# Performance work log

Hardware: AMD Instinct MI355X
Metric: run time of the kernel (lower is better)

## Reference

```python
import jax, jax.numpy as jnp
import numpy as np
from jax import lax

NQ = 9          # num_qubits
K = 3           # basis_size
S = 16          # max_num_snapshots
H = 128         # hidden_size
B = 16          # batch
D = 2 ** NQ

# basis_reconstruction buffer = Pauli X, Y, Z (complex64), non-trainable
PAULI = jnp.array([[[0, 1], [1, 0]],
                   [[0, -1j], [1j, 0]],
                   [[1, 0], [0, -1]]], dtype=jnp.complex64)


def setup_inputs() -> dict:
    key = jax.random.key(0)
    ks = jax.random.split(key, 11)
    return {
        "snapshot": jax.random.normal(ks[0], (B, NQ), jnp.float32),
        "basis_comp_vector": jax.random.uniform(ks[1], (B, NQ, K), dtype=jnp.float32),
        "rho": jax.random.normal(ks[2], (B, 2) + (2,) * NQ, jnp.float32),
        "h0": jax.random.normal(ks[3], (B, H), jnp.float32),
        "c0": jax.random.normal(ks[4], (B, H), jnp.float32),
        "W_ih": jax.random.normal(ks[5], (4 * H, NQ + NQ * K), jnp.float32) * 0.1,
        "W_hh": jax.random.normal(ks[6], (4 * H, H), jnp.float32) * 0.1,
        "b_ih": jax.random.normal(ks[7], (4 * H,), jnp.float32) * 0.1,
        "b_hh": jax.random.normal(ks[8], (4 * H,), jnp.float32) * 0.1,
        "Wp": jax.random.normal(ks[9], (NQ, K, H), jnp.float32) * 0.1,
        "bp": jax.random.normal(ks[10], (NQ, K), jnp.float32) * 0.1,
    }


def _lstm_cell(x, h, c, W_ih, W_hh, b_ih, b_hh):
    g = x @ W_ih.T + h @ W_hh.T + b_ih + b_hh
    i, f, gg, o = jnp.split(g, 4, axis=-1)  # torch gate order i,f,g,o
    i, f, o = jax.nn.sigmoid(i), jax.nn.sigmoid(f), jax.nn.sigmoid(o)
    c = f * c + i * jnp.tanh(gg)
    return o * jnp.tanh(c), c


def _apply_1q(psi, M, i):
    """Apply per-batch 2x2 matrix M [B,2,2] to qubit i of psi [B]+[2]*NQ."""
    psi = jnp.moveaxis(psi, 1 + i, 1)
    sh = psi.shape
    out = jnp.einsum('bij,bjr->bir', M, psi.reshape(sh[0], 2, -1))
    return jnp.moveaxis(out.reshape(sh), 1, 1 + i)


def _take_snapshots(psi, a):
    """Vectorized take_snapshot: psi [B]+[2]*NQ complex, a [B,NQ,K] real (sqrt of probs).
    For each qubit build psi_plus/psi_minus projectors, record expectation
    s = <P+> - <P-> and collapse onto the (normalized) plus branch."""
    axs = tuple(range(1, NQ + 1))
    zeros = jnp.zeros(psi.shape[0], jnp.float32)
    ss = []
    for i in range(NQ):
        a1, a2, a3 = a[:, i, 0], a[:, i, 1], a[:, i, 2]
        an = jnp.sqrt(a1 * a1 + a2 * a2 + a3 * a3)
        nrm = 1.0 / jnp.sqrt(2.0 * an * (a3 + an))
        pp = jnp.stack([lax.complex(a3 + an, zeros), lax.complex(a1, a2)], axis=-1) * nrm[:, None]
        pm = jnp.stack([lax.complex(-a1, a2), lax.complex(a3 + an, zeros)], axis=-1) * nrm[:, None]
        Pp = pp[:, :, None] * jnp.conj(pp)[:, None, :]  # [B,2,2]
        Pm = pm[:, :, None] * jnp.conj(pm)[:, None, :]
        psi_p = _apply_1q(psi, Pp, i)
        psi_m = _apply_1q(psi, Pm, i)
        prob_p = jnp.sum(psi_p.real ** 2 + psi_p.imag ** 2, axis=axs)
        prob_m = jnp.sum(psi_m.real ** 2 + psi_m.imag ** 2, axis=axs)
        ss.append(prob_p - prob_m)
        psi = psi_p / jnp.sqrt(prob_p).reshape((-1,) + (1,) * NQ)  # collapse
    return jnp.stack(ss, axis=1)  # [B,NQ]


def _bkron(A, Bm):
    b, m, n = A.shape
    p, q = Bm.shape[1], Bm.shape[2]
    return (A[:, :, None, :, None] * Bm[:, None, :, None, :]).reshape(b, m * p, n * q)


def _forward(snapshot, basis_comp_vector, rho, h0, c0, W_ih, W_hh, b_ih, b_hh, Wp, bp):
    b = snapshot.shape[0]
    psi = lax.complex(rho[:, 0], rho[:, 1])  # [B]+[2]*NQ pure state
    x = jnp.concatenate([snapshot, basis_comp_vector.reshape(b, -1)], axis=-1)
    inputs = [x]
    h, c = h0, c0
    for _ in range(S - 1):
        h, c = _lstm_cell(x, h, c, W_ih, W_hh, b_ih, b_hh)
        probs = jax.nn.softmax(jnp.einsum('bh,nkh->bnk', h, Wp) + bp, axis=-1)
        amps = jnp.sqrt(probs)  # [B,NQ,K]
        snap = _take_snapshots(psi, amps)
        x = jnp.concatenate([snap, amps.reshape(b, -1)], axis=-1)
        inputs.append(x)
    # classical-shadow reconstruction, summed over snapshots
    I2 = jnp.eye(2, dtype=jnp.complex64)
    acc = jnp.zeros((b, D, D), jnp.complex64)
    last_bv = None
    for x in inputs:
        shadow = x[:, :NQ]                                   # [B,NQ]
        bv = x[:, NQ:].reshape(b, NQ, K)
        last_bv = bv
        basis = jnp.einsum('bnk,kij->bnij', bv.astype(jnp.complex64), PAULI)
        rho_q = (I2 + shadow[:, :, None, None].astype(jnp.complex64) * basis * 3.0) / 2.0
        r = rho_q[:, 0]
        for iq in range(1, NQ):
            r = _bkron(r, rho_q[:, iq])
        acc = acc + r
    rho_rec = acc / S
    out = jnp.stack([rho_rec.real, rho_rec.imag], axis=1)  # [B,2,D,D]
    return out, last_bv


def reference(snapshot, basis_comp_vector, rho, h0, c0, W_ih, W_hh, b_ih, b_hh, Wp, bp):
    return _forward(snapshot, basis_comp_vector, rho, h0, c0,
                    W_ih, W_hh, b_ih, b_hh, Wp, bp)
```

## Files before the change

kernel.cpp:

```cpp
#include <hip/hip_runtime.h>
#include <math.h>

#define NQ 9
#define KK 3
#define S 16
#define H 128
#define BB 16
#define D 512
#define DD (D*D)

typedef float vfloat4 __attribute__((ext_vector_type(4)));

__device__ __forceinline__ float sigf(float x){ return 1.f/(1.f + __expf(-x)); }
__device__ __forceinline__ float tanhfast(float x){
  float e = __expf(2.f*x);
  return 1.f - 2.f/(e + 1.f);
}
#define RCP(x)  __builtin_amdgcn_rcpf(x)
#define RSQ(x)  __builtin_amdgcn_rsqf(x)

#define DPP_ADD(x, ctrl, rmask) \
  x += __int_as_float(__builtin_amdgcn_update_dpp(0, __float_as_int(x), ctrl, rmask, 0xf, false))

__device__ __forceinline__ float wave_red_sum(float x) {
  DPP_ADD(x, 0x111, 0xf);
  DPP_ADD(x, 0x112, 0xf);
  DPP_ADD(x, 0x114, 0xf);
  DPP_ADD(x, 0x118, 0xf);
  DPP_ADD(x, 0x142, 0xa);
  DPP_ADD(x, 0x143, 0xc);
  return __int_as_float(__builtin_amdgcn_readlane(__float_as_int(x), 63));
}
#define RL(v, l) __int_as_float(__builtin_amdgcn_readlane(__float_as_int(v), (l)))
#define DPP_ROR(x, n) \
  __int_as_float(__builtin_amdgcn_update_dpp(0, __float_as_int(x), 0x120 + (n), 0xf, 0xf, false))

__device__ __forceinline__ float ghh_rl4(const float4 (&whh)[32],
                                         float h0v, float h1v, float bias) {
  float g0 = bias, g1 = 0.f, g2 = 0.f, g3 = 0.f;
  #pragma unroll
  for (int j = 0; j < 32; ++j) {
    float4 wv = whh[j];
    g0 += wv.x*RL(h0v, 2*j);
    g1 += wv.y*RL(h1v, 2*j);
    g2 += wv.z*RL(h0v, 2*j + 1);
    g3 += wv.w*RL(h1v, 2*j + 1);
  }
  return (g0 + g1) + (g2 + g3);
}

__global__ __launch_bounds__(512, 2)
void seq_kernel(const float* __restrict__ snapshot,
                const float* __restrict__ bcv,
                const float* __restrict__ rho,
                const float* __restrict__ h0,
                const float* __restrict__ c0,
                const float* __restrict__ W_ih,
                const float* __restrict__ W_hh,
                const float* __restrict__ b_ih,
                const float* __restrict__ b_hh,
                const float* __restrict__ Wp,
                const float* __restrict__ bp,
                float4* __restrict__ mats,
                float* __restrict__ last_bv)
{
  const int b    = blockIdx.x;
  const int tid  = threadIdx.x;
  const int lane = tid & 63;
  const int w    = tid >> 6;

  __shared__ __align__(16) float xh[36];
  __shared__ float gbuf[512];
  __shared__ float prj[27];

  float4 wih[9], whh[32];
  {
    const float4* wi = (const float4*)(W_ih + tid*36);
    #pragma unroll
    for (int k = 0; k < 9; ++k) wih[k] = wi[k];
    const float4* wh = (const float4*)(W_hh + tid*H);
    #pragma unroll
    for (int k = 0; k < 32; ++k) whh[k] = wh[k];
  }
  const float bias = b_ih[tid] + b_hh[tid];

  float2 wpv[4]; float bpv[4];
  #pragma unroll
  for (int i = 0; i < 4; ++i) {
    int u = (w >= 1) ? (w - 1) + 7*i : 99;
    if (u < 27) { wpv[i] = *(const float2*)(Wp + u*H + 2*lane); bpv[i] = bp[u]; }
    else        { wpv[i] = make_float2(0.f, 0.f); bpv[i] = 0.f; }
  }

  float cc0 = c0[b*H + 2*lane], cc1 = c0[b*H + 2*lane + 1];
  float h0v = h0[b*H + 2*lane], h1v = h0[b*H + 2*lane + 1];

  float pr0[8], pi0[8], norm0 = 0.f;
  if (w == 0) {
    #pragma unroll
    for (int j = 0; j < 8; ++j) {
      pr0[j] = rho[b*1024 + j*64 + lane];
      pi0[j] = rho[b*1024 + 512 + j*64 + lane];
    }
    float ls = 0.f;
    #pragma unroll
    for (int j = 0; j < 8; ++j) ls += pr0[j]*pr0[j] + pi0[j]*pi0[j];
    norm0 = wave_red_sum(ls);
  }

  if (tid < NQ)  xh[tid]      = snapshot[b*NQ + tid];
  if (tid < 27)  xh[NQ + tid] = bcv[b*27 + tid];
  if (tid < NQ) {
    float s  = snapshot[b*NQ + tid];
    float v0 = bcv[b*27 + tid*3];
    float v1 = bcv[b*27 + tid*3 + 1];
    float v2 = bcv[b*27 + tid*3 + 2];
    mats[(b*S + 0)*NQ + tid] = make_float4(
        0.5f*(1.f + 3.f*s*v2), 1.5f*s*v0, -1.5f*s*v1, 0.5f*(1.f - 3.f*s*v2));
  }
  __syncthreads();

  float ghh = ghh_rl4(whh, h0v, h1v, bias);

  for (int t = 1; t < S; ++t) {
    {
      const float4* x4 = (const float4*)xh;
      float g0 = ghh, g1 = 0.f, g2 = 0.f, g3 = 0.f;
      #pragma unroll
      for (int k = 0; k < 9; ++k) {
        float4 wv = wih[k], xv = x4[k];
        g0 += wv.x*xv.x; g1 += wv.y*xv.y; g2 += wv.z*xv.z; g3 += wv.w*xv.w;
      }
      gbuf[tid] = (g0 + g1) + (g2 + g3);
    }
    __syncthreads();

    {
      float2 gI = *(const float2*)(gbuf + 2*lane);
      float2 gF = *(const float2*)(gbuf + 128 + 2*lane);
      float2 gG = *(const float2*)(gbuf + 256 + 2*lane);
      float2 gO = *(const float2*)(gbuf + 384 + 2*lane);
      cc0 = sigf(gF.x)*cc0 + sigf(gI.x)*tanhfast(gG.x);
      cc1 = sigf(gF.y)*cc1 + sigf(gI.y)*tanhfast(gG.y);
      h0v = sigf(gO.x)*tanhfast(cc0);
      h1v = sigf(gO.y)*tanhfast(cc1);
    }
    if (w > 0) {
      #pragma unroll
      for (int i = 0; i < 4; ++i) {
        float p = wave_red_sum(wpv[i].x*h0v + wpv[i].y*h1v);
        int u = (w - 1) + 7*i;
        if (u < 27 && lane == 0) prj[u] = p + bpv[i];
      }
    } else if (t < S - 1) {
      ghh = ghh_rl4(whh, h0v, h1v, bias);
    }
    __syncthreads();

    if (w == 0) {
      float a1 = 0.f, a2 = 0.f, a3 = 0.f;
      float k0v = 0.f, k1rv = 0.f, k1iv = 0.f;
      if (lane < NQ) {
        float l0 = prj[lane*3], l1 = prj[lane*3+1], l2 = prj[lane*3+2];
        float mx = fmaxf(l0, fmaxf(l1, l2));
        float e0 = __expf(l0 - mx), e1 = __expf(l1 - mx), e2 = __expf(l2 - mx);
        float inv = RCP(e0 + e1 + e2);
        a1 = sqrtf(e0*inv); a2 = sqrtf(e1*inv); a3 = sqrtf(e2*inv);
        float an = sqrtf(a1*a1 + a2*a2 + a3*a3);
        float t3 = a3 + an;
        float n1 = RSQ(2.f*an*t3);
        k0v = n1*t3; k1rv = n1*a1; k1iv = -n1*a2;
      }
      float part[9];

      float r4[4], i4[4];
      {
        const float K0 = RL(k0v,0), K1r = RL(k1rv,0), K1i = RL(k1iv,0);
        float lp = 0.f;
        #pragma unroll
        for (int j = 0; j < 4; ++j) {
          r4[j] = K0*pr0[j] + K1r*pr0[j+4] - K1i*pi0[j+4];
          i4[j] = K0*pi0[j] + K1r*pi0[j+4] + K1i*pr0[j+4];
          lp += r4[j]*r4[j] + i4[j]*i4[j];
        }
        part[0] = lp;
      }
      float r2[2], i2[2];
      {
        const float K0 = RL(k0v,1), K1r = RL(k1rv,1), K1i = RL(k1iv,1);
        float lp = 0.f;
        #pragma unroll
        for (int j = 0; j < 2; ++j) {
          r2[j] = K0*r4[j] + K1r*r4[j+2] - K1i*i4[j+2];
          i2[j] = K0*i4[j] + K1r*i4[j+2] + K1i*r4[j+2];
          lp += r2[j]*r2[j] + i2[j]*i2[j];
        }
        part[1] = lp;
      }
      float wr, wi_;
      {
        const float K0 = RL(k0v,2), K1r = RL(k1rv,2), K1i = RL(k1iv,2);
        wr  = K0*r2[0] + K1r*r2[1] - K1i*i2[1];
        wi_ = K0*i2[0] + K1r*i2[1] + K1i*r2[1];
        part[2] = wr*wr + wi_*wi_;
      }
      #pragma unroll
      for (int q = 3; q < 5; ++q) {
        const int half = 32 >> (q - 3);
        const float K0 = RL(k0v,q), K1r = RL(k1rv,q), K1i = RL(k1iv,q);
        float pr = __shfl(wr,  lane + half, 64);
        float pi = __shfl(wi_, lane + half, 64);
        float nr = K0*wr  + K1r*pr - K1i*pi;
        float ni = K0*wi_ + K1r*pi + K1i*pr;
        wr = nr; wi_ = ni;
        part[q] = (lane < half) ? (nr*nr + ni*ni) : 0.f;
      }
      #pragma unroll
      for (int q = 5; q < NQ; ++q) {
        const int half = 32 >> (q - 3);
        const float K0 = RL(k0v,q), K1r = RL(k1rv,q), K1i = RL(k1iv,q);
        float pr, pi;
        if      (q == 5) { pr = DPP_ROR(wr, 8);  pi = DPP_ROR(wi_, 8);  }
        else if (q == 6) { pr = DPP_ROR(wr, 12); pi = DPP_ROR(wi_, 12); }
        else if (q == 7) { pr = DPP_ROR(wr, 14); pi = DPP_ROR(wi_, 14); }
        else             { pr = DPP_ROR(wr, 15); pi = DPP_ROR(wi_, 15); }
        float nr = K0*wr  + K1r*pr - K1i*pi;
        float ni = K0*wi_ + K1r*pi + K1i*pr;
        wr = nr; wi_ = ni;
        part[q] = (lane < half) ? (nr*nr + ni*ni) : 0.f;
      }
      float L[9];
      #pragma unroll
      for (int q = 0; q < NQ; ++q) L[q] = wave_red_sum(part[q]);
      float sv = 2.f*L[0] - norm0;
      #pragma unroll
      for (int q = 1; q < NQ; ++q) {
        float r = 2.f*L[q]*RCP(L[q-1]) - 1.f;
        sv = (lane == q) ? r : sv;
      }
      if (lane < NQ) {
        xh[lane] = sv;
        xh[9 + lane*3]     = a1;
        xh[9 + lane*3 + 1] = a2;
        xh[9 + lane*3 + 2] = a3;
        mats[(b*S + t)*NQ + lane] = make_float4(
            0.5f*(1.f + 3.f*sv*a3), 1.5f*sv*a1,
            -1.5f*sv*a2,            0.5f*(1.f - 3.f*sv*a3));
      }
    } else if (t < S - 1) {
      ghh = ghh_rl4(whh, h0v, h1v, bias);
    }
    __syncthreads();
  }

  if (tid < 27) last_bv[b*27 + tid] = xh[9 + tid];
}

__device__ __forceinline__ void herm_entry(float4 m, int rb, int cb, float& er, float& ei) {
  if (rb == 0) { if (cb == 0) { er = m.x; ei = 0.f; } else { er = m.y; ei = m.z; } }
  else         { if (cb == 0) { er = m.y; ei = -m.z; } else { er = m.w; ei = 0.f; } }
}

__device__ __forceinline__ void nt_store4(float* p, float x, float y, float z, float w) {
  vfloat4 v; v.x = x; v.y = y; v.z = z; v.w = w;
  __builtin_nontemporal_store(v, (vfloat4*)p);
}

__global__ __launch_bounds__(512, 2)
void kron_kernel(const float4* __restrict__ mats_g, float* __restrict__ out)
{
  const int b   = blockIdx.y;
  const int bm  = blockIdx.x;
  const int tid = threadIdx.x;
  const int rTp = bm >> 3;
  const int rg  = bm & 7;

  __shared__ float4 matsh[S*NQ];
  __shared__ float2 top[S][2][16];
  __shared__ __align__(16) float2 bot[4][S][32];

  if (tid < S*NQ) matsh[tid] = mats_g[b*S*NQ + tid];
  __syncthreads();

  {
    int t = tid >> 5, rTi = (tid >> 4) & 1, cT = tid & 15;
    int rT = rTp*2 + rTi;
    float re = 1.f, im = 0.f;
    #pragma unroll
    for (int q = 0; q < 4; ++q) {
      int rb = (rT >> (3 - q)) & 1, cb = (cT >> (3 - q)) & 1;
      float er, ei; herm_entry(matsh[t*NQ + q], rb, cb, er, ei);
      float nr = re*er - im*ei; im = re*ei + im*er; re = nr;
    }
    top[t][rTi][cT] = make_float2(re, im);
  }
  #pragma unroll
  for (int i = 0; i < 4; ++i) {
    int n  = tid + 512*i;
    int r_ = n >> 9, t_ = (n >> 5) & 15, cB = n & 31;
    int rB = rg*4 + r_;
    float re = 1.f, im = 0.f;
    #pragma unroll
    for (int q = 0; q < 5; ++q) {
      int rb = (rB >> (4 - q)) & 1, cb = (cB >> (4 - q)) & 1;
      float er, ei; herm_entry(matsh[t_*NQ + 4 + q], rb, cb, er, ei);
      float nr = re*er - im*ei; im = re*ei + im*er; re = nr;
    }
    bot[r_][t_][cB] = make_float2(re, im);
  }
  __syncthreads();

  const int rb = tid >> 7;
  const int c0 = (tid & 127) << 2;
  const int cT = c0 >> 5, cB = c0 & 31;
  float4 a0r = make_float4(0,0,0,0), a0i = make_float4(0,0,0,0);
  float4 a1r = make_float4(0,0,0,0), a1i = make_float4(0,0,0,0);
  #pragma unroll
  for (int t = 0; t < S; ++t) {
    float4 b01 = *(const float4*)&bot[rb][t][cB];
    float4 b23 = *(const float4*)&bot[rb][t][cB + 2];
    float2 tA = top[t][0][cT];
    float2 tB = top[t][1][cT];
    a0r.x += tA.x*b01.x - tA.y*b01.y;  a0i.x += tA.x*b01.y + tA.y*b01.x;
    a0r.y += tA.x*b01.z - tA.y*b01.w;  a0i.y += tA.x*b01.w + tA.y*b01.z;
    a0r.z += tA.x*b23.x - tA.y*b23.y;  a0i.z += tA.x*b23.y + tA.y*b23.x;
    a0r.w += tA.x*b23.z - tA.y*b23.w;  a0i.w += tA.x*b23.w + tA.y*b23.z;
    a1r.x += tB.x*b01.x - tB.y*b01.y;  a1i.x += tB.x*b01.y + tB.y*b01.x;
    a1r.y += tB.x*b01.z - tB.y*b01.w;  a1i.y += tB.x*b01.w + tB.y*b01.z;
    a1r.z += tB.x*b23.x - tB.y*b23.y;  a1i.z += tB.x*b23.y + tB.y*b23.x;
    a1r.w += tB.x*b23.z - tB.y*b23.w;  a1i.w += tB.x*b23.w + tB.y*b23.z;
  }
  const float invS = 1.f/16.f;
  const int rowA = (rTp*2)*32 + rg*4 + rb;
  const int rowB = rowA + 32;
  size_t baseA = ((size_t)b*2)*DD + (size_t)rowA*D + c0;
  size_t baseB = ((size_t)b*2)*DD + (size_t)rowB*D + c0;
  nt_store4(out + baseA,      a0r.x*invS, a0r.y*invS, a0r.z*invS, a0r.w*invS);
  nt_store4(out + baseA + DD, a0i.x*invS, a0i.y*invS, a0i.z*invS, a0i.w*invS);
  nt_store4(out + baseB,      a1r.x*invS, a1r.y*invS, a1r.z*invS, a1r.w*invS);
  nt_store4(out + baseB + DD, a1i.x*invS, a1i.y*invS, a1i.z*invS, a1i.w*invS);
}

extern "C" void kernel_launch(void* const* d_in, const int* in_sizes, int n_in,
                              void* d_out, int out_size, void* d_ws, size_t ws_size,
                              hipStream_t stream) {
  const float* snapshot = (const float*)d_in[0];
  const float* bcv      = (const float*)d_in[1];
  const float* rho      = (const float*)d_in[2];
  const float* h0       = (const float*)d_in[3];
  const float* c0       = (const float*)d_in[4];
  const float* W_ih     = (const float*)d_in[5];
  const float* W_hh     = (const float*)d_in[6];
  const float* b_ih     = (const float*)d_in[7];
  const float* b_hh     = (const float*)d_in[8];
  const float* Wp       = (const float*)d_in[9];
  const float* bp       = (const float*)d_in[10];

  float*  out     = (float*)d_out;
  float4* mats    = (float4*)d_ws;
  float*  last_bv = out + (size_t)BB*2*DD;

  seq_kernel<<<BB, 512, 0, stream>>>(snapshot, bcv, rho, h0, c0,
                                     W_ih, W_hh, b_ih, b_hh, Wp, bp,
                                     mats, last_bv);

  dim3 grid(64, BB);
  kron_kernel<<<grid, 512, 0, stream>>>(mats, out);
}
```

Before: 152.0 us.

## Move per-qubit softmax and Kraus coefficient computation into projection waves

The Wp projection weights are staged in LDS, and each non-zero wave now owns whole qubits: it computes all three logits, the softmax, the amplitudes and the collapse coefficients, then writes them to a small shared table. Wave 0 no longer runs the serial softmax after the barrier and reads the coefficients from LDS instead of through readlane. This shortens the critical path inside the sequential 16-step loop. In exchange it uses about 14 KB more shared memory, does more wave reductions per wave, and puts an uneven load on waves 1-2.

```diff
diff --git a/kernel.cpp b/kernel.cpp
--- a/kernel.cpp
+++ b/kernel.cpp
@@ -47,6 +47,36 @@
     g3 += wv.w*RL(h1v, 2*j + 1);
   }
   return (g0 + g1) + (g2 + g3);
+}
+
+__device__ __forceinline__ void qubit_owner(int q, int lane,
+                                            float h0v, float h1v,
+                                            const float* wp_lds,
+                                            const float* bp_lds,
+                                            float (*kb)[6], float* xh) {
+  float l0, l1, l2;
+  {
+    const float2 w0 = *(const float2*)&wp_lds[(3*q    )*H + 2*lane];
+    const float2 w1 = *(const float2*)&wp_lds[(3*q + 1)*H + 2*lane];
+    const float2 w2 = *(const float2*)&wp_lds[(3*q + 2)*H + 2*lane];
+    l0 = wave_red_sum(w0.x*h0v + w0.y*h1v) + bp_lds[3*q];
+    l1 = wave_red_sum(w1.x*h0v + w1.y*h1v) + bp_lds[3*q + 1];
+    l2 = wave_red_sum(w2.x*h0v + w2.y*h1v) + bp_lds[3*q + 2];
+  }
+  float mx = fmaxf(l0, fmaxf(l1, l2));
+  float e0 = __expf(l0 - mx), e1 = __expf(l1 - mx), e2 = __expf(l2 - mx);
+  float inv = RCP(e0 + e1 + e2);
+  float a1 = sqrtf(e0*inv), a2 = sqrtf(e1*inv), a3 = sqrtf(e2*inv);
+  float an = sqrtf(a1*a1 + a2*a2 + a3*a3);
+  float t3 = a3 + an;
+  float n1 = RSQ(2.f*an*t3);
+  if (lane == 0) {
+    kb[q][0] = n1*t3; kb[q][1] = n1*a1; kb[q][2] = -n1*a2;
+    kb[q][3] = a1;    kb[q][4] = a2;    kb[q][5] = a3;
+    xh[9 + 3*q]     = a1;
+    xh[9 + 3*q + 1] = a2;
+    xh[9 + 3*q + 2] = a3;
+  }
 }
 
 __global__ __launch_bounds__(512, 2)
@@ -71,7 +101,9 @@
 
   __shared__ __align__(16) float xh[36];
   __shared__ float gbuf[512];
-  __shared__ float prj[27];
+  __shared__ __align__(16) float wp_lds[27*H];
+  __shared__ float bp_lds[27];
+  __shared__ float kb[NQ][6];
 
   float4 wih[9], whh[32];
   {
@@ -84,13 +116,8 @@
   }
   const float bias = b_ih[tid] + b_hh[tid];
 
-  float2 wpv[4]; float bpv[4];
-  #pragma unroll
-  for (int i = 0; i < 4; ++i) {
-    int u = (w >= 1) ? (w - 1) + 7*i : 99;
-    if (u < 27) { wpv[i] = *(const float2*)(Wp + u*H + 2*lane); bpv[i] = bp[u]; }
-    else        { wpv[i] = make_float2(0.f, 0.f); bpv[i] = 0.f; }
-  }
+  for (int idx = tid; idx < 27*H; idx += 512) wp_lds[idx] = Wp[idx];
+  if (tid < 27) bp_lds[tid] = bp[tid];
 
   float cc0 = c0[b*H + 2*lane], cc1 = c0[b*H + 2*lane + 1];
   float h0v = h0[b*H + 2*lane], h1v = h0[b*H + 2*lane + 1];
@@ -146,36 +173,19 @@
       h1v = sigf(gO.y)*tanhfast(cc1);
     }
     if (w > 0) {
-      #pragma unroll
-      for (int i = 0; i < 4; ++i) {
-        float p = wave_red_sum(wpv[i].x*h0v + wpv[i].y*h1v);
-        int u = (w - 1) + 7*i;
-        if (u < 27 && lane == 0) prj[u] = p + bpv[i];
-      }
+      qubit_owner(w - 1, lane, h0v, h1v, wp_lds, bp_lds, kb, xh);
+      if (w <= 2) qubit_owner(w + 6, lane, h0v, h1v, wp_lds, bp_lds, kb, xh);
     } else if (t < S - 1) {
       ghh = ghh_rl4(whh, h0v, h1v, bias);
     }
     __syncthreads();
 
     if (w == 0) {
-      float a1 = 0.f, a2 = 0.f, a3 = 0.f;
-      float k0v = 0.f, k1rv = 0.f, k1iv = 0.f;
-      if (lane < NQ) {
-        float l0 = prj[lane*3], l1 = prj[lane*3+1], l2 = prj[lane*3+2];
-        float mx = fmaxf(l0, fmaxf(l1, l2));
-        float e0 = __expf(l0 - mx), e1 = __expf(l1 - mx), e2 = __expf(l2 - mx);
-        float inv = RCP(e0 + e1 + e2);
-        a1 = sqrtf(e0*inv); a2 = sqrtf(e1*inv); a3 = sqrtf(e2*inv);
-        float an = sqrtf(a1*a1 + a2*a2 + a3*a3);
-        float t3 = a3 + an;
-        float n1 = RSQ(2.f*an*t3);
-        k0v = n1*t3; k1rv = n1*a1; k1iv = -n1*a2;
-      }
       float part[9];
 
       float r4[4], i4[4];
       {
-        const float K0 = RL(k0v,0), K1r = RL(k1rv,0), K1i = RL(k1iv,0);
+        const float K0 = kb[0][0], K1r = kb[0][1], K1i = kb[0][2];
         float lp = 0.f;
         #pragma unroll
         for (int j = 0; j < 4; ++j) {
@@ -187,7 +197,7 @@
       }
       float r2[2], i2[2];
       {
-        const float K0 = RL(k0v,1), K1r = RL(k1rv,1), K1i = RL(k1iv,1);
+        const float K0 = kb[1][0], K1r = kb[1][1], K1i = kb[1][2];
         float lp = 0.f;
         #pragma unroll
         for (int j = 0; j < 2; ++j) {
@@ -199,7 +209,7 @@
       }
       float wr, wi_;
       {
-        const float K0 = RL(k0v,2), K1r = RL(k1rv,2), K1i = RL(k1iv,2);
+        const float K0 = kb[2][0], K1r = kb[2][1], K1i = kb[2][2];
         wr  = K0*r2[0] + K1r*r2[1] - K1i*i2[1];
         wi_ = K0*i2[0] + K1r*i2[1] + K1i*r2[1];
         part[2] = wr*wr + wi_*wi_;
@@ -207,7 +217,7 @@
       #pragma unroll
       for (int q = 3; q < 5; ++q) {
         const int half = 32 >> (q - 3);
-        const float K0 = RL(k0v,q), K1r = RL(k1rv,q), K1i = RL(k1iv,q);
+        const float K0 = kb[q][0], K1r = kb[q][1], K1i = kb[q][2];
         float pr = __shfl(wr,  lane + half, 64);
         float pi = __shfl(wi_, lane + half, 64);
         float nr = K0*wr  + K1r*pr - K1i*pi;
@@ -218,7 +228,7 @@
       #pragma unroll
       for (int q = 5; q < NQ; ++q) {
         const int half = 32 >> (q - 3);
-        const float K0 = RL(k0v,q), K1r = RL(k1rv,q), K1i = RL(k1iv,q);
+        const float K0 = kb[q][0], K1r = kb[q][1], K1i = kb[q][2];
         float pr, pi;
         if      (q == 5) { pr = DPP_ROR(wr, 8);  pi = DPP_ROR(wi_, 8);  }
         else if (q == 6) { pr = DPP_ROR(wr, 12); pi = DPP_ROR(wi_, 12); }
@@ -239,13 +249,11 @@
         sv = (lane == q) ? r : sv;
       }
       if (lane < NQ) {
+        float A1 = kb[lane][3], A2 = kb[lane][4], A3 = kb[lane][5];
         xh[lane] = sv;
-        xh[9 + lane*3]     = a1;
-        xh[9 + lane*3 + 1] = a2;
-        xh[9 + lane*3 + 2] = a3;
         mats[(b*S + t)*NQ + lane] = make_float4(
-            0.5f*(1.f + 3.f*sv*a3), 1.5f*sv*a1,
-            -1.5f*sv*a2,            0.5f*(1.f - 3.f*sv*a3));
+            0.5f*(1.f + 3.f*sv*A3), 1.5f*sv*A1,
+            -1.5f*sv*A2,            0.5f*(1.f - 3.f*sv*A3));
       }
     } else if (t < S - 1) {
       ghh = ghh_rl4(whh, h0v, h1v, bias);
```

New measurement: 154.4 us. No clear change (+1.6%).
